# Optimization experiments

Hardware: AMD Instinct MI355X
Metric: run time of the kernel (lower is better)

Reference implementation:

```python
import jax, jax.numpy as jnp
import numpy as np
from jax import lax

EPS = 1e-5

def _conv3x3(x, w, stride=1):
    # x: [B,C,H,W], w: [O,I,3,3]
    dn = lax.conv_dimension_numbers(x.shape, w.shape, ('NCHW', 'OIHW', 'NCHW'))
    return lax.conv_general_dilated(x, w, window_strides=(stride, stride),
                                    padding=((1, 1), (1, 1)), dimension_numbers=dn)

def _batchnorm(x, gamma, beta):
    # training-mode BN over (N,H,W) per channel
    mean = jnp.mean(x, axis=(0, 2, 3), keepdims=True)
    var = jnp.var(x, axis=(0, 2, 3), keepdims=True)
    inv = lax.rsqrt(var + EPS)
    return (x - mean) * inv * gamma[None, :, None, None] + beta[None, :, None, None]

def setup_inputs() -> dict:
    key = jax.random.key(0)
    ks = jax.random.split(key, 8)
    B, C, H, W, E = 16, 256, 64, 64, 512
    x = jax.random.normal(ks[0], (B, C, H, W), dtype=jnp.float32)
    embedding = jax.random.normal(ks[1], (B, E), dtype=jnp.float32)
    s_conv = 1.0 / np.sqrt(C * 9)
    conv1_w = jax.random.normal(ks[2], (C, C, 3, 3), dtype=jnp.float32) * s_conv
    conv2_w = jax.random.normal(ks[3], (C, C, 3, 3), dtype=jnp.float32) * s_conv
    s_g = 1.0 / np.sqrt(E)
    g1_w = jax.random.normal(ks[4], (E, C), dtype=jnp.float32) * s_g
    g1_b = jnp.zeros((C,), dtype=jnp.float32)
    g2_w = jax.random.normal(ks[5], (E, C), dtype=jnp.float32) * s_g
    g2_b = jnp.zeros((C,), dtype=jnp.float32)
    bn1_g = jnp.ones((C,), dtype=jnp.float32)
    bn1_b = jnp.zeros((C,), dtype=jnp.float32)
    bn2_g = jnp.ones((C,), dtype=jnp.float32)
    bn2_b = jnp.zeros((C,), dtype=jnp.float32)
    return {"x": x, "embedding": embedding, "conv1_w": conv1_w, "conv2_w": conv2_w,
            "g1_w": g1_w, "g1_b": g1_b, "g2_w": g2_w, "g2_b": g2_b,
            "bn1_g": bn1_g, "bn1_b": bn1_b, "bn2_g": bn2_g, "bn2_b": bn2_b}

def reference(x, embedding, conv1_w, conv2_w, g1_w, g1_b, g2_w, g2_b,
              bn1_g, bn1_b, bn2_g, bn2_b):
    identity = x
    # gate 1: per-sample per-channel gate values (softmax over channels)
    gate1 = jax.nn.softmax(embedding @ g1_w + g1_b, axis=-1)  # [B,C]
    out = _conv3x3(x, conv1_w, stride=1) * gate1[:, :, None, None]
    out = jax.nn.relu(_batchnorm(out, bn1_g, bn1_b))
    # gate 2
    gate2 = jax.nn.softmax(embedding @ g2_w + g2_b, axis=-1)  # [B,C]
    out = _conv3x3(out, conv2_w, stride=1) * gate2[:, :, None, None]
    out = _batchnorm(out, bn2_g, bn2_b)
    out = jax.nn.relu(out + identity)
    return (out, gate1, gate2)
```

## Files before the change

kernel.cpp:

```cpp
#include <hip/hip_runtime.h>

typedef __attribute__((ext_vector_type(8))) short short8;
typedef __attribute__((ext_vector_type(4))) float f32x4;

#define HP 66

__device__ __forceinline__ unsigned short f2bf(float f) {
  unsigned u = __builtin_bit_cast(unsigned, f);
  u += 0x7FFFu + ((u >> 16) & 1u);
  return (unsigned short)(u >> 16);
}
__device__ __forceinline__ float bf2f(unsigned short h) {
  return __builtin_bit_cast(float, ((unsigned)h) << 16);
}
__device__ __forceinline__ __attribute__((address_space(3))) void* to_as3(void* p) {
  return (__attribute__((address_space(3))) void*)(unsigned)(unsigned long long)p;
}
__device__ __forceinline__ const __attribute__((address_space(1))) void* to_as1(const void* p) {
  return (const __attribute__((address_space(1))) void*)(unsigned long long)p;
}

#define SB0() __builtin_amdgcn_sched_barrier(0)
#define BAR() do { SB0(); __builtin_amdgcn_s_barrier(); SB0(); } while (0)

__global__ __launch_bounds__(256) void k_prep(
    const float* __restrict__ x, unsigned short* __restrict__ xp,
    const float* __restrict__ w1, const float* __restrict__ w2,
    unsigned short* __restrict__ wT1, unsigned short* __restrict__ wT2,
    const float* __restrict__ emb,
    const float* __restrict__ g1w, const float* __restrict__ g1b,
    const float* __restrict__ g2w, const float* __restrict__ g2b,
    float* __restrict__ gate1, float* __restrict__ gate2) {
  __shared__ float tile[32][65];
  __shared__ float ebuf[512];
  __shared__ float red[8];
  const int blk = blockIdx.x;
  const int t = threadIdx.x;

  if (blk < 8192) {
    int ct = blk & 7, h = (blk >> 3) & 63, b = blk >> 9;
    int c0 = ct * 32;
    int w = t & 63, cs = t >> 6;
#pragma unroll
    for (int i = 0; i < 8; ++i) {
      int c = cs + i * 4;
      tile[c][w] = x[(((b * 256) + c0 + c) * 64 + h) * 64 + w];
    }
    __syncthreads();
    int cl = (t & 15) * 2, w0 = t >> 4;
#pragma unroll
    for (int i = 0; i < 4; ++i) {
      int ww = w0 + i * 16;
      unsigned v = (unsigned)f2bf(tile[cl][ww]) | ((unsigned)f2bf(tile[cl + 1][ww]) << 16);
      *(unsigned*)(xp + ((long)((b*HP + h + 1)*HP + (ww + 1)) * 256 + c0 + cl)) = v;
    }
  } else if (blk < 10272) {
    unsigned u = (unsigned)(blk - 8192) * 256 + t;
    unsigned p_idx = u >> 7, word = u & 127;
    int img = p_idx / 260, p = p_idx % 260;
    int h, w;
    if (p < 66)      { h = 0;  w = p; }
    else if (p < 132){ h = 65; w = p - 66; }
    else             { int q = p - 132; h = 1 + (q >> 1); w = (q & 1) * 65; }
    ((unsigned*)xp)[((long)((img*HP + h)*HP + w) * 256) / 2 + word] = 0u;
  } else if (blk < 10784) {
    int idx = blk - 10272;
    const float* w = (idx >> 8) ? w2 : w1;
    unsigned short* wT = (idx >> 8) ? wT2 : wT1;
    int co = idx & 255;
#pragma unroll
    for (int kk = 0; kk < 9; ++kk)
      wT[co * 2304 + kk * 256 + t] = f2bf(w[(co * 256 + t) * 9 + kk]);
  } else {
    int idx = blk - 10784;
    int b = idx & 15;
    const float* gw = (idx >> 4) ? g2w : g1w;
    const float* gbias = (idx >> 4) ? g2b : g1b;
    float* gout = (idx >> 4) ? gate2 : gate1;
    ebuf[t] = emb[b * 512 + t];
    ebuf[t + 256] = emb[b * 512 + t + 256];
    __syncthreads();
    float acc = gbias[t];
    for (int k = 0; k < 512; ++k) acc += ebuf[k] * gw[k * 256 + t];
    float mx = acc;
    for (int off = 32; off >= 1; off >>= 1) mx = fmaxf(mx, __shfl_xor(mx, off));
    if ((t & 63) == 0) red[t >> 6] = mx;
    __syncthreads();
    mx = fmaxf(fmaxf(red[0], red[1]), fmaxf(red[2], red[3]));
    float e = expf(acc - mx);
    float sm = e;
    for (int off = 32; off >= 1; off >>= 1) sm += __shfl_xor(sm, off);
    if ((t & 63) == 0) red[4 + (t >> 6)] = sm;
    __syncthreads();
    sm = red[4] + red[5] + red[6] + red[7];
    gout[b * 256 + t] = e / sm;
  }
}

__global__ __launch_bounds__(256, 2) void k_conv(
    const unsigned short* __restrict__ inp,
    const unsigned short* __restrict__ wT,
    const float* __restrict__ gate,
    unsigned short* __restrict__ yout,
    float* __restrict__ partials) {
  __shared__ short As[2][128][64];
  __shared__ short Bs[2][128][64];
  __shared__ float sbuf[2][128][2];

  const int t = threadIdx.x;
  const int lane = t & 63;
  const int wid = t >> 6;
  const int wm = wid >> 1;
  const int wn = wid & 1;
  const int lr = lane & 15;
  const int hi = lane >> 4;
  const int key = lr & 7;

  const int blk = ((blockIdx.x & 7) << 7) + (blockIdx.x >> 3);
  const int mt = blk >> 1;
  const int nt = blk & 1;
  const int b = mt >> 5;
  const int hh2 = (mt & 31) << 1;

  const int r0 = t >> 3;
  const int cdst = (t & 7) << 3;
  const int cg8 = (((t & 7) ^ ((t >> 3) & 7)) << 3);

  int aoff[4];
#pragma unroll
  for (int i = 0; i < 4; ++i)
    aoff[i] = (b * HP + hh2 + (i >> 1)) * HP + (r0 + 32 * (i & 1));

  auto stageA_h = [&](int buf, int h, int s) {
    int kk = s >> 2;
    int kh = (kk * 11) >> 5;
    int khw = kh * 66 + (kk - kh * 3);
    int ci = ((s & 3) << 6) + cg8;
    const unsigned short* g0 = inp + (long)(aoff[h] + khw) * 256 + ci;
    const unsigned short* g1 = inp + (long)(aoff[2 + h] + khw) * 256 + ci;
    __builtin_amdgcn_global_load_lds(to_as1(g0), to_as3((void*)&As[buf][h * 32 + r0][cdst]), 16, 0, 0);
    __builtin_amdgcn_global_load_lds(to_as1(g1), to_as3((void*)&As[buf][64 + h * 32 + r0][cdst]), 16, 0, 0);
  };
  auto stageB_h = [&](int buf, int h, int s) {
    int co = nt * 128 + h * 32 + r0;
    const unsigned short* g0 = wT + (long)co * 2304 + s * 64 + cg8;
    const unsigned short* g1 = wT + (long)(co + 64) * 2304 + s * 64 + cg8;
    __builtin_amdgcn_global_load_lds(to_as1(g0), to_as3((void*)&Bs[buf][h * 32 + r0][cdst]), 16, 0, 0);
    __builtin_amdgcn_global_load_lds(to_as1(g1), to_as3((void*)&Bs[buf][64 + h * 32 + r0][cdst]), 16, 0, 0);
  };

  f32x4 acc[4][4];
#pragma unroll
  for (int i = 0; i < 4; ++i)
#pragma unroll
    for (int j = 0; j < 4; ++j) acc[i][j] = (f32x4){0.f, 0.f, 0.f, 0.f};

  short8 afrag0[2][2], afrag1[2][2];
  short8 bfrag0[2][2], bfrag1[2][2];

#define RD_A(ARR, AH, BUF)                                                           \
  _Pragma("unroll") for (int mf = 0; mf < 2; ++mf)                                   \
    _Pragma("unroll") for (int ks = 0; ks < 2; ++ks)                                 \
      ARR[mf][ks] = *(const short8*)&As[BUF][wm * 64 + (AH) * 32 + mf * 16 + lr][((ks * 4 + hi) ^ key) << 3];
#define RD_B(ARR, NH, BUF)                                                           \
  _Pragma("unroll") for (int nf = 0; nf < 2; ++nf)                                   \
    _Pragma("unroll") for (int ks = 0; ks < 2; ++ks)                                 \
      ARR[nf][ks] = *(const short8*)&Bs[BUF][wn * 64 + (NH) * 32 + nf * 16 + lr][((ks * 4 + hi) ^ key) << 3];

#define QUADQ(AF, BF, mh, nh)                                                        \
  do {                                                                               \
    __builtin_amdgcn_s_setprio(1);                                                   \
    _Pragma("unroll") for (int ks = 0; ks < 2; ++ks)                                 \
      _Pragma("unroll") for (int mo = 0; mo < 2; ++mo)                               \
        _Pragma("unroll") for (int no = 0; no < 2; ++no)                             \
          acc[(mh) * 2 + mo][(nh) * 2 + no] = __builtin_amdgcn_mfma_f32_16x16x32_bf16( \
              AF[mo][ks], BF[no][ks], acc[(mh) * 2 + mo][(nh) * 2 + no], 0, 0, 0);   \
    __builtin_amdgcn_s_setprio(0);                                                   \
  } while (0)

  stageA_h(0, 0, 0); stageB_h(0, 0, 0); stageA_h(0, 1, 0); stageB_h(0, 1, 0);
  stageA_h(1, 0, 1); stageB_h(1, 0, 1); stageA_h(1, 1, 1); stageB_h(1, 1, 1);
  asm volatile("s_waitcnt vmcnt(8)" ::: "memory");
  BAR();
  RD_B(bfrag0, 0, 0);
  RD_A(afrag0, 0, 0);

#define KTHALF2(SEL, kt)                                                             \
  {                                                                                  \
    RD_B(bfrag1, 1, SEL);                                                            \
    RD_A(afrag1, 1, SEL);                                                            \
    SB0();                                                                           \
    QUADQ(afrag0, bfrag0, 0, 0);                                                     \
    QUADQ(afrag0, bfrag1, 0, 1);                                                     \
    QUADQ(afrag1, bfrag0, 1, 0);                                                     \
    if ((kt) < 35) { asm volatile("s_waitcnt vmcnt(4)" ::: "memory"); }              \
    BAR();                                                                           \
    if ((kt) < 35) { RD_B(bfrag0, 0, SEL ^ 1); RD_A(afrag0, 0, SEL ^ 1); }           \
    if ((kt) + 2 < 36) { stageA_h(SEL, 0, (kt) + 2); stageB_h(SEL, 0, (kt) + 2);     \
                         stageA_h(SEL, 1, (kt) + 2); stageB_h(SEL, 1, (kt) + 2); }   \
    SB0();                                                                           \
    QUADQ(afrag1, bfrag1, 1, 1);                                                     \
    if ((kt) < 34)      { asm volatile("s_waitcnt vmcnt(8)" ::: "memory"); }         \
    else if ((kt) == 34){ asm volatile("s_waitcnt vmcnt(0)" ::: "memory"); }         \
    BAR();                                                                           \
  }

  for (int i = 0; i < 18; ++i) {
    const int kt0 = 2 * i;
    KTHALF2(0, kt0)
    KTHALF2(1, kt0 + 1)
  }
#undef KTHALF2
#undef QUADQ
#undef RD_A
#undef RD_B

  float g[4];
#pragma unroll
  for (int nf = 0; nf < 4; ++nf)
    g[nf] = gate[(b << 8) + nt * 128 + wn * 64 + nf * 16 + lr];

  float s[4] = {0, 0, 0, 0}, sq[4] = {0, 0, 0, 0};
  const int mrow0 = mt * 128 + wm * 64 + (hi << 2);
  const int c0 = nt * 128 + wn * 64 + lr;
#pragma unroll
  for (int mf = 0; mf < 4; ++mf)
#pragma unroll
    for (int r = 0; r < 4; ++r) {
      const int mm = mrow0 + mf * 16 + r;
#pragma unroll
      for (int nf = 0; nf < 4; ++nf) {
        float v = acc[mf][nf][r] * g[nf];
        yout[(long)mm * 256 + c0 + nf * 16] = f2bf(v);
        s[nf] += v;
        sq[nf] += v * v;
      }
    }
#pragma unroll
  for (int nf = 0; nf < 4; ++nf) {
    s[nf] += __shfl_xor(s[nf], 16);  s[nf] += __shfl_xor(s[nf], 32);
    sq[nf] += __shfl_xor(sq[nf], 16); sq[nf] += __shfl_xor(sq[nf], 32);
  }
  if (hi == 0) {
#pragma unroll
    for (int nf = 0; nf < 4; ++nf) {
      int c = wn * 64 + nf * 16 + lr;
      sbuf[wm][c][0] = s[nf];
      sbuf[wm][c][1] = sq[nf];
    }
  }
  __syncthreads();
  if (t < 128) {
    partials[mt * 256 + nt * 128 + t]          = sbuf[0][t][0] + sbuf[1][t][0];
    partials[131072 + mt * 256 + nt * 128 + t] = sbuf[0][t][1] + sbuf[1][t][1];
  }
}

__global__ __launch_bounds__(256) void k_bnfin(const float* __restrict__ partials,
                                               const float* __restrict__ gamma,
                                               const float* __restrict__ beta,
                                               float2* __restrict__ aff) {
  __shared__ float red[8];
  int c = blockIdx.x, t = threadIdx.x;
  float s  = partials[t * 256 + c]          + partials[(t + 256) * 256 + c];
  float sq = partials[131072 + t * 256 + c] + partials[131072 + (t + 256) * 256 + c];
  for (int off = 32; off >= 1; off >>= 1) { s += __shfl_xor(s, off); sq += __shfl_xor(sq, off); }
  if ((t & 63) == 0) { red[t >> 6] = s; red[4 + (t >> 6)] = sq; }
  __syncthreads();
  if (t == 0) {
    s = red[0] + red[1] + red[2] + red[3];
    sq = red[4] + red[5] + red[6] + red[7];
    float mean = s * (1.0f / 65536.0f);
    float var = fmaxf(sq * (1.0f / 65536.0f) - mean * mean, 0.0f);
    float inv = rsqrtf(var + 1e-5f);
    float ga = gamma[c] * inv;
    aff[c] = make_float2(ga, beta[c] - mean * ga);
  }
}

__global__ __launch_bounds__(256) void k_mid(const unsigned short* __restrict__ y1,
                                             const float2* __restrict__ aff,
                                             unsigned short* __restrict__ zp) {
  long idx = (long)blockIdx.x * 256 + threadIdx.x;
  int c0 = (int)(idx & 31) * 8;
  long pos = idx >> 5;
  int b = (int)(pos >> 12), hw = (int)(pos & 4095);
  int h = hw >> 6, w = hw & 63;
  uint4 v = *(const uint4*)(y1 + pos * 256 + c0);
  unsigned vv[4] = {v.x, v.y, v.z, v.w};
  unsigned outp[4];
#pragma unroll
  for (int j = 0; j < 4; ++j) {
    float2 aL = aff[c0 + 2 * j], aH = aff[c0 + 2 * j + 1];
    float lo = fmaxf(aL.x * bf2f((unsigned short)(vv[j] & 0xFFFF)) + aL.y, 0.f);
    float hiv = fmaxf(aH.x * bf2f((unsigned short)(vv[j] >> 16)) + aH.y, 0.f);
    outp[j] = (unsigned)f2bf(lo) | ((unsigned)f2bf(hiv) << 16);
  }
  unsigned short* dst = zp + (long)((b * HP + h + 1) * HP + w + 1) * 256 + c0;
  *(uint4*)dst = make_uint4(outp[0], outp[1], outp[2], outp[3]);
}

__global__ __launch_bounds__(256) void k_final(const unsigned short* __restrict__ y2,
                                               const float2* __restrict__ aff,
                                               const float* __restrict__ x,
                                               float* __restrict__ out) {
  __shared__ float tile[64][33];
  int blk = blockIdx.x;
  int ct = blk & 7, h = (blk >> 3) & 63, b = blk >> 9;
  int c0 = ct * 32;
  int t = threadIdx.x;
  int cl = (t & 15) * 2, w0 = t >> 4;
#pragma unroll
  for (int i = 0; i < 4; ++i) {
    int w = w0 + i * 16;
    unsigned v = *(const unsigned*)(y2 + (long)((b * 4096) + h * 64 + w) * 256 + c0 + cl);
    float2 aL = aff[c0 + cl], aH = aff[c0 + cl + 1];
    tile[w][cl] = aL.x * bf2f((unsigned short)(v & 0xFFFF)) + aL.y;
    tile[w][cl + 1] = aH.x * bf2f((unsigned short)(v >> 16)) + aH.y;
  }
  __syncthreads();
  int w = t & 63, csub = t >> 6;
#pragma unroll
  for (int j = 0; j < 8; ++j) {
    int c = c0 + csub * 8 + j;
    long o = ((long)(b * 256 + c) * 64 + h) * 64 + w;
    out[o] = fmaxf(tile[w][csub * 8 + j] + x[o], 0.f);
  }
}

extern "C" void kernel_launch(void* const* d_in, const int* in_sizes, int n_in,
                              void* d_out, int out_size, void* d_ws, size_t ws_size,
                              hipStream_t stream) {
  const float* x    = (const float*)d_in[0];
  const float* emb  = (const float*)d_in[1];
  const float* w1   = (const float*)d_in[2];
  const float* w2   = (const float*)d_in[3];
  const float* g1w  = (const float*)d_in[4];
  const float* g1b  = (const float*)d_in[5];
  const float* g2w  = (const float*)d_in[6];
  const float* g2b  = (const float*)d_in[7];
  const float* bn1g = (const float*)d_in[8];
  const float* bn1b = (const float*)d_in[9];
  const float* bn2g = (const float*)d_in[10];
  const float* bn2b = (const float*)d_in[11];

  float* out = (float*)d_out;
  float* gate1 = out + 16777216;
  float* gate2 = gate1 + 4096;

  char* ws = (char*)d_ws;
  const size_t OFF_XP  = 0;
  const size_t OFF_WT1 = 35684352;
  const size_t OFF_WT2 = OFF_WT1 + 1179648;
  const size_t OFF_Y   = OFF_WT2 + 1179648;
  const size_t OFF_PART = OFF_Y + 33554432;
  const size_t OFF_AFF1 = OFF_PART + 2097152;
  const size_t OFF_AFF2 = OFF_AFF1 + 2048;

  unsigned short* xp  = (unsigned short*)(ws + OFF_XP);
  unsigned short* wT1 = (unsigned short*)(ws + OFF_WT1);
  unsigned short* wT2 = (unsigned short*)(ws + OFF_WT2);
  unsigned short* y   = (unsigned short*)(ws + OFF_Y);
  float* part = (float*)(ws + OFF_PART);
  float2* aff1 = (float2*)(ws + OFF_AFF1);
  float2* aff2 = (float2*)(ws + OFF_AFF2);

  k_prep<<<10816, 256, 0, stream>>>(x, xp, w1, w2, wT1, wT2, emb,
                                    g1w, g1b, g2w, g2b, gate1, gate2);

  k_conv<<<1024, 256, 0, stream>>>(xp, wT1, gate1, y, part);
  k_bnfin<<<256, 256, 0, stream>>>(part, bn1g, bn1b, aff1);
  k_mid<<<8192, 256, 0, stream>>>(y, aff1, xp);

  k_conv<<<1024, 256, 0, stream>>>(xp, wT2, gate2, y, part);
  k_bnfin<<<256, 256, 0, stream>>>(part, bn2g, bn2b, aff2);
  k_final<<<8192, 256, 0, stream>>>(y, aff2, x, out);
}
```

Measured before the change: 238.1 us.

## Warp-specialize conv kernel with producer loader waves and LDS flag handshakes

Restructures the implicit-GEMM conv kernel into two producer waves that stage A/B tiles into LDS with global_load_lds, and four consumer waves that run the MFMA loop. Block-wide barriers are replaced by LDS atomic ready/done counters with spin-waits. The goal is to decouple memory staging from compute so the MFMA waves no longer stall on barriers and vmcnt waits. The costs are 384 threads per block with a target occupancy of 3 blocks, polling with s_sleep, and producers that fully drain vmcnt after every tile, which limits prefetch depth to the two buffers.

```diff
diff --git a/kernel.cpp b/kernel.cpp
--- a/kernel.cpp
+++ b/kernel.cpp
@@ -19,9 +19,6 @@
 __device__ __forceinline__ const __attribute__((address_space(1))) void* to_as1(const void* p) {
   return (const __attribute__((address_space(1))) void*)(unsigned long long)p;
 }
-
-#define SB0() __builtin_amdgcn_sched_barrier(0)
-#define BAR() do { SB0(); __builtin_amdgcn_s_barrier(); SB0(); } while (0)
 
 __global__ __launch_bounds__(256) void k_prep(
     const float* __restrict__ x, unsigned short* __restrict__ xp,
@@ -97,7 +94,7 @@
   }
 }
 
-__global__ __launch_bounds__(256, 2) void k_conv(
+__global__ __launch_bounds__(384, 3) void k_conv(
     const unsigned short* __restrict__ inp,
     const unsigned short* __restrict__ wT,
     const float* __restrict__ gate,
@@ -106,12 +103,12 @@
   __shared__ short As[2][128][64];
   __shared__ short Bs[2][128][64];
   __shared__ float sbuf[2][128][2];
+  __shared__ int rdy[2];
+  __shared__ int done[2];
 
   const int t = threadIdx.x;
   const int lane = t & 63;
   const int wid = t >> 6;
-  const int wm = wid >> 1;
-  const int wn = wid & 1;
   const int lr = lane & 15;
   const int hi = lane >> 4;
   const int key = lr & 7;
@@ -122,131 +119,137 @@
   const int b = mt >> 5;
   const int hh2 = (mt & 31) << 1;
 
-  const int r0 = t >> 3;
-  const int cdst = (t & 7) << 3;
-  const int cg8 = (((t & 7) ^ ((t >> 3) & 7)) << 3);
-
-  int aoff[4];
+  if (t == 0) { rdy[0] = 0; rdy[1] = 0; done[0] = 0; done[1] = 0; }
+  __syncthreads();
+
+  auto waitge = [&](int* p, int v) {
+    while (__hip_atomic_load(p, __ATOMIC_ACQUIRE, __HIP_MEMORY_SCOPE_WORKGROUP) < v)
+      __builtin_amdgcn_s_sleep(1);
+  };
+  auto signal = [&](int* p) {
+    if (lane == 0)
+      __hip_atomic_fetch_add(p, 1, __ATOMIC_RELEASE, __HIP_MEMORY_SCOPE_WORKGROUP);
+  };
+
+  f32x4 acc[4][4];
 #pragma unroll
   for (int i = 0; i < 4; ++i)
-    aoff[i] = (b * HP + hh2 + (i >> 1)) * HP + (r0 + 32 * (i & 1));
-
-  auto stageA_h = [&](int buf, int h, int s) {
-    int kk = s >> 2;
-    int kh = (kk * 11) >> 5;
-    int khw = kh * 66 + (kk - kh * 3);
-    int ci = ((s & 3) << 6) + cg8;
-    const unsigned short* g0 = inp + (long)(aoff[h] + khw) * 256 + ci;
-    const unsigned short* g1 = inp + (long)(aoff[2 + h] + khw) * 256 + ci;
-    __builtin_amdgcn_global_load_lds(to_as1(g0), to_as3((void*)&As[buf][h * 32 + r0][cdst]), 16, 0, 0);
-    __builtin_amdgcn_global_load_lds(to_as1(g1), to_as3((void*)&As[buf][64 + h * 32 + r0][cdst]), 16, 0, 0);
-  };
-  auto stageB_h = [&](int buf, int h, int s) {
-    int co = nt * 128 + h * 32 + r0;
-    const unsigned short* g0 = wT + (long)co * 2304 + s * 64 + cg8;
-    const unsigned short* g1 = wT + (long)(co + 64) * 2304 + s * 64 + cg8;
-    __builtin_amdgcn_global_load_lds(to_as1(g0), to_as3((void*)&Bs[buf][h * 32 + r0][cdst]), 16, 0, 0);
-    __builtin_amdgcn_global_load_lds(to_as1(g1), to_as3((void*)&Bs[buf][64 + h * 32 + r0][cdst]), 16, 0, 0);
-  };
-
-  f32x4 acc[4][4];
-#pragma unroll
-  for (int i = 0; i < 4; ++i)
 #pragma unroll
     for (int j = 0; j < 4; ++j) acc[i][j] = (f32x4){0.f, 0.f, 0.f, 0.f};
 
-  short8 afrag0[2][2], afrag1[2][2];
-  short8 bfrag0[2][2], bfrag1[2][2];
-
-#define RD_A(ARR, AH, BUF)                                                           \
-  _Pragma("unroll") for (int mf = 0; mf < 2; ++mf)                                   \
-    _Pragma("unroll") for (int ks = 0; ks < 2; ++ks)                                 \
-      ARR[mf][ks] = *(const short8*)&As[BUF][wm * 64 + (AH) * 32 + mf * 16 + lr][((ks * 4 + hi) ^ key) << 3];
-#define RD_B(ARR, NH, BUF)                                                           \
-  _Pragma("unroll") for (int nf = 0; nf < 2; ++nf)                                   \
-    _Pragma("unroll") for (int ks = 0; ks < 2; ++ks)                                 \
-      ARR[nf][ks] = *(const short8*)&Bs[BUF][wn * 64 + (NH) * 32 + nf * 16 + lr][((ks * 4 + hi) ^ key) << 3];
-
-#define QUADQ(AF, BF, mh, nh)                                                        \
-  do {                                                                               \
-    __builtin_amdgcn_s_setprio(1);                                                   \
-    _Pragma("unroll") for (int ks = 0; ks < 2; ++ks)                                 \
-      _Pragma("unroll") for (int mo = 0; mo < 2; ++mo)                               \
-        _Pragma("unroll") for (int no = 0; no < 2; ++no)                             \
-          acc[(mh) * 2 + mo][(nh) * 2 + no] = __builtin_amdgcn_mfma_f32_16x16x32_bf16( \
-              AF[mo][ks], BF[no][ks], acc[(mh) * 2 + mo][(nh) * 2 + no], 0, 0, 0);   \
-    __builtin_amdgcn_s_setprio(0);                                                   \
-  } while (0)
-
-  stageA_h(0, 0, 0); stageB_h(0, 0, 0); stageA_h(0, 1, 0); stageB_h(0, 1, 0);
-  stageA_h(1, 0, 1); stageB_h(1, 0, 1); stageA_h(1, 1, 1); stageB_h(1, 1, 1);
-  asm volatile("s_waitcnt vmcnt(8)" ::: "memory");
-  BAR();
-  RD_B(bfrag0, 0, 0);
-  RD_A(afrag0, 0, 0);
-
-#define KTHALF2(SEL, kt)                                                             \
-  {                                                                                  \
-    RD_B(bfrag1, 1, SEL);                                                            \
-    RD_A(afrag1, 1, SEL);                                                            \
-    SB0();                                                                           \
-    QUADQ(afrag0, bfrag0, 0, 0);                                                     \
-    QUADQ(afrag0, bfrag1, 0, 1);                                                     \
-    QUADQ(afrag1, bfrag0, 1, 0);                                                     \
-    if ((kt) < 35) { asm volatile("s_waitcnt vmcnt(4)" ::: "memory"); }              \
-    BAR();                                                                           \
-    if ((kt) < 35) { RD_B(bfrag0, 0, SEL ^ 1); RD_A(afrag0, 0, SEL ^ 1); }           \
-    if ((kt) + 2 < 36) { stageA_h(SEL, 0, (kt) + 2); stageB_h(SEL, 0, (kt) + 2);     \
-                         stageA_h(SEL, 1, (kt) + 2); stageB_h(SEL, 1, (kt) + 2); }   \
-    SB0();                                                                           \
-    QUADQ(afrag1, bfrag1, 1, 1);                                                     \
-    if ((kt) < 34)      { asm volatile("s_waitcnt vmcnt(8)" ::: "memory"); }         \
-    else if ((kt) == 34){ asm volatile("s_waitcnt vmcnt(0)" ::: "memory"); }         \
-    BAR();                                                                           \
-  }
-
-  for (int i = 0; i < 18; ++i) {
-    const int kt0 = 2 * i;
-    KTHALF2(0, kt0)
-    KTHALF2(1, kt0 + 1)
-  }
-#undef KTHALF2
-#undef QUADQ
-#undef RD_A
-#undef RD_B
-
-  float g[4];
-#pragma unroll
-  for (int nf = 0; nf < 4; ++nf)
-    g[nf] = gate[(b << 8) + nt * 128 + wn * 64 + nf * 16 + lr];
-
-  float s[4] = {0, 0, 0, 0}, sq[4] = {0, 0, 0, 0};
-  const int mrow0 = mt * 128 + wm * 64 + (hi << 2);
-  const int c0 = nt * 128 + wn * 64 + lr;
-#pragma unroll
-  for (int mf = 0; mf < 4; ++mf)
-#pragma unroll
-    for (int r = 0; r < 4; ++r) {
-      const int mm = mrow0 + mf * 16 + r;
+  if (wid >= 4) {
+    const int pt = t - 256;
+    const int prow = pt >> 3;
+    const int pch = pt & 7;
+    const int cg8p = ((pch ^ (prow & 7)) << 3);
+
+    int abase[8];
+#pragma unroll
+    for (int i = 0; i < 8; ++i) {
+      int arow = i * 16 + prow;
+      abase[i] = (b * HP + hh2 + (arow >> 6)) * HP + (arow & 63);
+    }
+
+    auto stageTile = [&](int buf, int s) {
+      int kk = s >> 2;
+      int kh = (kk * 11) >> 5;
+      int khw = kh * 66 + (kk - kh * 3);
+      int ci = ((s & 3) << 6) + cg8p;
+#pragma unroll
+      for (int i = 0; i < 8; ++i) {
+        const unsigned short* g = inp + (long)(abase[i] + khw) * 256 + ci;
+        __builtin_amdgcn_global_load_lds(to_as1(g), to_as3((void*)&As[buf][i * 16 + prow][pch << 3]), 16, 0, 0);
+      }
+#pragma unroll
+      for (int i = 0; i < 8; ++i) {
+        const unsigned short* g = wT + (long)(nt * 128 + i * 16 + prow) * 2304 + s * 64 + cg8p;
+        __builtin_amdgcn_global_load_lds(to_as1(g), to_as3((void*)&Bs[buf][i * 16 + prow][pch << 3]), 16, 0, 0);
+      }
+    };
+
+    stageTile(0, 0);
+    stageTile(1, 1);
+    asm volatile("s_waitcnt vmcnt(0)" ::: "memory");
+    signal(&rdy[0]);
+    signal(&rdy[1]);
+
+    for (int s = 2; s < 36; ++s) {
+      const int bb = s & 1;
+      waitge(&done[bb], 4 * (s >> 1));
+      stageTile(bb, s);
+      asm volatile("s_waitcnt vmcnt(0)" ::: "memory");
+      signal(&rdy[bb]);
+    }
+  } else {
+    const int wm = wid >> 1;
+    const int wn = wid & 1;
+
+#define CONS_KT(SEL, kt)                                                             \
+    {                                                                                \
+      waitge(&rdy[SEL], 2 * (((kt) >> 1) + 1));                                      \
+      short8 af[4][2], bf[4][2];                                                     \
+      _Pragma("unroll") for (int mf = 0; mf < 4; ++mf)                               \
+        _Pragma("unroll") for (int ks = 0; ks < 2; ++ks)                             \
+          af[mf][ks] = *(const short8*)&As[SEL][wm * 64 + mf * 16 + lr][((ks * 4 + hi) ^ key) << 3]; \
+      _Pragma("unroll") for (int nf = 0; nf < 4; ++nf)                               \
+        _Pragma("unroll") for (int ks = 0; ks < 2; ++ks)                             \
+          bf[nf][ks] = *(const short8*)&Bs[SEL][wn * 64 + nf * 16 + lr][((ks * 4 + hi) ^ key) << 3]; \
+      __builtin_amdgcn_s_setprio(1);                                                 \
+      _Pragma("unroll") for (int ks = 0; ks < 2; ++ks)                               \
+        _Pragma("unroll") for (int mf = 0; mf < 4; ++mf)                             \
+          _Pragma("unroll") for (int nf = 0; nf < 4; ++nf)                           \
+            acc[mf][nf] = __builtin_amdgcn_mfma_f32_16x16x32_bf16(                   \
+                af[mf][ks], bf[nf][ks], acc[mf][nf], 0, 0, 0);                       \
+      __builtin_amdgcn_s_setprio(0);                                                 \
+      signal(&done[SEL]);                                                            \
+    }
+
+    for (int i = 0; i < 18; ++i) {
+      const int kt0 = 2 * i;
+      CONS_KT(0, kt0)
+      CONS_KT(1, kt0 + 1)
+    }
+#undef CONS_KT
+  }
+
+  __syncthreads();
+
+  if (wid < 4) {
+    const int wm = wid >> 1;
+    const int wn = wid & 1;
+    float g[4];
+#pragma unroll
+    for (int nf = 0; nf < 4; ++nf)
+      g[nf] = gate[(b << 8) + nt * 128 + wn * 64 + nf * 16 + lr];
+
+    float s[4] = {0, 0, 0, 0}, sq[4] = {0, 0, 0, 0};
+    const int mrow0 = mt * 128 + wm * 64 + (hi << 2);
+    const int c0 = nt * 128 + wn * 64 + lr;
+#pragma unroll
+    for (int mf = 0; mf < 4; ++mf)
+#pragma unroll
+      for (int r = 0; r < 4; ++r) {
+        const int mm = mrow0 + mf * 16 + r;
+#pragma unroll
+        for (int nf = 0; nf < 4; ++nf) {
+          float v = acc[mf][nf][r] * g[nf];
+          yout[(long)mm * 256 + c0 + nf * 16] = f2bf(v);
+          s[nf] += v;
+          sq[nf] += v * v;
+        }
+      }
+#pragma unroll
+    for (int nf = 0; nf < 4; ++nf) {
+      s[nf] += __shfl_xor(s[nf], 16);  s[nf] += __shfl_xor(s[nf], 32);
+      sq[nf] += __shfl_xor(sq[nf], 16); sq[nf] += __shfl_xor(sq[nf], 32);
+    }
+    if (hi == 0) {
 #pragma unroll
       for (int nf = 0; nf < 4; ++nf) {
-        float v = acc[mf][nf][r] * g[nf];
-        yout[(long)mm * 256 + c0 + nf * 16] = f2bf(v);
-        s[nf] += v;
-        sq[nf] += v * v;
+        int c = wn * 64 + nf * 16 + lr;
+        sbuf[wm][c][0] = s[nf];
+        sbuf[wm][c][1] = sq[nf];
       }
-    }
-#pragma unroll
-  for (int nf = 0; nf < 4; ++nf) {
-    s[nf] += __shfl_xor(s[nf], 16);  s[nf] += __shfl_xor(s[nf], 32);
-    sq[nf] += __shfl_xor(sq[nf], 16); sq[nf] += __shfl_xor(sq[nf], 32);
-  }
-  if (hi == 0) {
-#pragma unroll
-    for (int nf = 0; nf < 4; ++nf) {
-      int c = wn * 64 + nf * 16 + lr;
-      sbuf[wm][c][0] = s[nf];
-      sbuf[wm][c][1] = sq[nf];
     }
   }
   __syncthreads();
@@ -368,11 +371,11 @@
   k_prep<<<10816, 256, 0, stream>>>(x, xp, w1, w2, wT1, wT2, emb,
                                     g1w, g1b, g2w, g2b, gate1, gate2);
 
-  k_conv<<<1024, 256, 0, stream>>>(xp, wT1, gate1, y, part);
+  k_conv<<<1024, 384, 0, stream>>>(xp, wT1, gate1, y, part);
   k_bnfin<<<256, 256, 0, stream>>>(part, bn1g, bn1b, aff1);
   k_mid<<<8192, 256, 0, stream>>>(y, aff1, xp);
 
-  k_conv<<<1024, 256, 0, stream>>>(xp, wT2, gate2, y, part);
+  k_conv<<<1024, 384, 0, stream>>>(xp, wT2, gate2, y, part);
   k_bnfin<<<256, 256, 0, stream>>>(part, bn2g, bn2b, aff2);
   k_final<<<8192, 256, 0, stream>>>(y, aff2, x, out);
 }
```

Result: slower. 328.4 us (+37.9%).
